# Optimization experiments

Hardware: AMD Instinct MI355X
Metric: run time of the kernel (lower is better)

## Reference

```python
import jax, jax.numpy as jnp
import numpy as np

B, LP, LM = 16, 128, 256      # batch, persona len, msg len
V, E, H = 32000, 512, 512     # vocab, embed dim, lstm units
DENC = 2 * H                  # bidirectional encoder output width


def _glorot(key, shape):
    return jax.random.normal(key, shape, jnp.float32) * (1.0 / np.sqrt(shape[0]))


def setup_inputs() -> dict:
    key = jax.random.key(0)
    ks = jax.random.split(key, 32)
    d = {}
    d["input_word"] = jax.random.randint(ks[0], (B, 1), 0, V)
    d["enc_persona"] = jax.random.normal(ks[1], (B, LP, DENC), jnp.float32)
    d["enc_msg"] = jax.random.normal(ks[2], (B, LM, DENC), jnp.float32)
    d["ctx"] = jax.random.normal(ks[3], (B, 2 * DENC), jnp.float32)
    for i, n in enumerate(["h1", "c1", "h2", "c2", "h3", "c3", "h4", "c4"]):
        d[n] = jax.random.normal(ks[4 + i], (B, H), jnp.float32) * 0.1
    d["emb_table"] = jax.random.normal(ks[12], (V, E), jnp.float32) * 0.02
    in_sizes = [E + 2 * DENC, H, H, H]
    k = 13
    for li, sz in enumerate(in_sizes, start=1):
        d[f"lstm{li}_Wx"] = _glorot(ks[k], (sz, 4 * H)); k += 1
        d[f"lstm{li}_Wh"] = _glorot(ks[k], (H, 4 * H)); k += 1
        d[f"lstm{li}_b"] = jnp.zeros((4 * H,), jnp.float32)
    for pre in ["p", "m"]:
        d[f"{pre}W1_w"] = _glorot(ks[k], (DENC, H)); k += 1
        d[f"{pre}W1_b"] = jnp.zeros((H,), jnp.float32)
        d[f"{pre}W2_w"] = _glorot(ks[k], (H, H)); k += 1
        d[f"{pre}W2_b"] = jnp.zeros((H,), jnp.float32)
        d[f"{pre}V_w"] = _glorot(ks[k], (H, 1)); k += 1
        d[f"{pre}V_b"] = jnp.zeros((1,), jnp.float32)
    d["out_w"] = _glorot(ks[k], (H + 2 * DENC, V)); k += 1
    d["out_b"] = jnp.zeros((V,), jnp.float32)
    return d


def _lstm_step(x, h, c, Wx, Wh, b):
    # Keras LSTM gate order: i, f, g (candidate), o
    z = x @ Wx + h @ Wh + b
    i, f, g, o = jnp.split(z, 4, axis=-1)
    c_new = jax.nn.sigmoid(f) * c + jax.nn.sigmoid(i) * jnp.tanh(g)
    h_new = jax.nn.sigmoid(o) * jnp.tanh(c_new)
    return h_new, c_new


def _bahdanau(enc, dec, W1w, W1b, W2w, W2b, Vw, Vb):
    # enc: [B, L, DENC], dec: [B, 1, H]
    score = jnp.tanh(enc @ W1w + W1b + dec @ W2w + W2b) @ Vw + Vb  # [B, L, 1]
    w = jax.nn.softmax(score, axis=1)
    ctx = jnp.sum(w * enc, axis=1)  # [B, DENC]
    return ctx, w


def reference(input_word, enc_persona, enc_msg, ctx, h1, c1, h2, c2, h3, c3, h4, c4,
              emb_table,
              lstm1_Wx, lstm1_Wh, lstm1_b, lstm2_Wx, lstm2_Wh, lstm2_b,
              lstm3_Wx, lstm3_Wh, lstm3_b, lstm4_Wx, lstm4_Wh, lstm4_b,
              pW1_w, pW1_b, pW2_w, pW2_b, pV_w, pV_b,
              mW1_w, mW1_b, mW2_w, mW2_b, mV_w, mV_b,
              out_w, out_b):
    emb = emb_table[input_word[:, 0]]                 # [B, E]
    x = jnp.concatenate([ctx, emb], axis=-1)          # [B, 2*DENC + E] (seq len 1, squeezed)
    h1, c1 = _lstm_step(x, h1, c1, lstm1_Wx, lstm1_Wh, lstm1_b)
    h2, c2 = _lstm_step(h1, h2, c2, lstm2_Wx, lstm2_Wh, lstm2_b)
    h3, c3 = _lstm_step(h2, h3, c3, lstm3_Wx, lstm3_Wh, lstm3_b)
    h4, c4 = _lstm_step(h3, h4, c4, lstm4_Wx, lstm4_Wh, lstm4_b)
    dec = h4[:, None, :]                              # [B, 1, H]
    p_ctx, p_w = _bahdanau(enc_persona, dec, pW1_w, pW1_b, pW2_w, pW2_b, pV_w, pV_b)
    m_ctx, m_w = _bahdanau(enc_msg, dec, mW1_w, mW1_b, mW2_w, mW2_b, mV_w, mV_b)
    ctx_new = jnp.concatenate([p_ctx, m_ctx], axis=-1)  # [B, 2*DENC]
    # dropout is identity at inference
    logits = jnp.concatenate([h4, ctx_new], axis=-1) @ out_w + out_b  # [B, V]
    return (logits, p_w, m_w, ctx_new, h1, c1, h2, c2, h3, c3, h4, c4)
```

## Files before the change

### kernel.cpp

```cpp
#include <hip/hip_runtime.h>
#include <hip/hip_bf16.h>

#define B 16
#define LP 128
#define LM 256
#define V 32000
#define E 512
#define H 512
#define DENC 1024
#define K1 2560
#define G4 2048

#define OFF_LOGITS 0
#define OFF_PW 512000
#define OFF_MW 514048
#define OFF_CTX 518144
#define OFF_H1 550912
#define OFF_C1 559104
#define OFF_H2 567296
#define OFF_C2 575488
#define OFF_H3 583680
#define OFF_C3 591872
#define OFF_H4 600064
#define OFF_C4 608256

#define ZSPLIT 32
#define LSPLIT 4

#define WS_X      0
#define WS_ZPART  40960
#define WS_D2P    1089536
#define WS_D2M    1097728
#define WS_SP     1105920
#define WS_SM     1107968
#define WS_XXT    1112064
#define WS_LPART  1153024

__device__ __forceinline__ float sigm(float x) { return 1.0f / (1.0f + expf(-x)); }

__global__ void k_embed(const int* __restrict__ word, const float* __restrict__ ctx,
                        const float* __restrict__ emb, float* __restrict__ x)
{
    int b = blockIdx.x;
    int w = word[b];
    for (int i = threadIdx.x; i < 2 * DENC; i += 256) x[b * K1 + i] = ctx[b * 2 * DENC + i];
    for (int i = threadIdx.x; i < E; i += 256)        x[b * K1 + 2 * DENC + i] = emb[(size_t)w * E + i];
}

__global__ void k_lstm_zp(const float* __restrict__ x, int kx,
                          const float* __restrict__ h,
                          const float* __restrict__ Wx, const float* __restrict__ Wh,
                          float* __restrict__ zpart)
{
    int j = blockIdx.x * 256 + threadIdx.x;
    int K = kx + H;
    int chunk = K / ZSPLIT;
    int k0 = blockIdx.y * chunk;
    int k1 = k0 + chunk;

    __shared__ float xs[96 * 16];
    for (int idx = threadIdx.x; idx < chunk * 16; idx += 256) {
        int kk = idx >> 4, b = idx & 15;
        int k = k0 + kk;
        xs[idx] = (k < kx) ? x[b * kx + k] : h[b * H + (k - kx)];
    }
    __syncthreads();

    float acc[16];
    #pragma unroll
    for (int b = 0; b < 16; ++b) acc[b] = 0.f;

    #pragma unroll 4
    for (int k = k0; k < k1; ++k) {
        float w = (k < kx) ? Wx[(size_t)k * G4 + j] : Wh[(size_t)(k - kx) * G4 + j];
        const float4* xp = (const float4*)&xs[(k - k0) * 16];
        float4 x0 = xp[0], x1 = xp[1], x2 = xp[2], x3 = xp[3];
        acc[0]  += x0.x * w; acc[1]  += x0.y * w; acc[2]  += x0.z * w; acc[3]  += x0.w * w;
        acc[4]  += x1.x * w; acc[5]  += x1.y * w; acc[6]  += x1.z * w; acc[7]  += x1.w * w;
        acc[8]  += x2.x * w; acc[9]  += x2.y * w; acc[10] += x2.z * w; acc[11] += x2.w * w;
        acc[12] += x3.x * w; acc[13] += x3.y * w; acc[14] += x3.z * w; acc[15] += x3.w * w;
    }

    float* zp = zpart + (size_t)blockIdx.y * B * G4;
    #pragma unroll
    for (int b = 0; b < 16; ++b) zp[b * G4 + j] = acc[b];
}

__global__ void k_gates(const float* __restrict__ zpart, const float* __restrict__ bias,
                        const float* __restrict__ c_old,
                        float* __restrict__ h_new, float* __restrict__ c_new)
{
    int b = blockIdx.y;
    int j = blockIdx.x * 256 + threadIdx.x;
    float zi = bias[j], zf = bias[H + j], zg = bias[2 * H + j], zo = bias[3 * H + j];
    #pragma unroll
    for (int s = 0; s < ZSPLIT; ++s) {
        const float* zp = zpart + ((size_t)s * B + b) * G4;
        zi += zp[j]; zf += zp[H + j]; zg += zp[2 * H + j]; zo += zp[3 * H + j];
    }
    float c = sigm(zf) * c_old[b * H + j] + sigm(zi) * tanhf(zg);
    float hh = sigm(zo) * tanhf(c);
    c_new[b * H + j] = c;
    h_new[b * H + j] = hh;
}

__global__ void k_decproj(const float* __restrict__ h4,
                          const float* __restrict__ pW2w, const float* __restrict__ pW2b,
                          const float* __restrict__ mW2w, const float* __restrict__ mW2b,
                          float* __restrict__ d2p, float* __restrict__ d2m)
{
    int b = blockIdx.y;
    int j = blockIdx.x * 256 + threadIdx.x;
    int which = blockIdx.z;
    const float* W = which ? mW2w : pW2w;
    const float* bb = which ? mW2b : pW2b;
    float* o = which ? d2m : d2p;
    const float* hr = h4 + b * H;
    float acc = bb[j];
    #pragma unroll 8
    for (int k = 0; k < H; ++k) acc += hr[k] * W[k * H + j];
    o[b * H + j] = acc;
}

#define TL 16
#define CH 128
__global__ void k_attscore(const float* __restrict__ encP, const float* __restrict__ encM,
                           const float* __restrict__ pW1w, const float* __restrict__ pW1b,
                           const float* __restrict__ pVw,  const float* __restrict__ pVb,
                           const float* __restrict__ mW1w, const float* __restrict__ mW1b,
                           const float* __restrict__ mVw,  const float* __restrict__ mVb,
                           const float* __restrict__ d2p,  const float* __restrict__ d2m,
                           float* __restrict__ sp, float* __restrict__ sm)
{
    __shared__ float smem[4352];
    int tile = blockIdx.x, b = blockIdx.y, tid = threadIdx.x;
    const int PT = LP / TL;
    const float *enc, *W1, *W1bv, *Vw, *Vbv, *d2;
    float* sout; int L, l0;
    if (tile < PT) { enc = encP; W1 = pW1w; W1bv = pW1b; Vw = pVw; Vbv = pVb; d2 = d2p; sout = sp; L = LP; l0 = tile * TL; }
    else           { enc = encM; W1 = mW1w; W1bv = mW1b; Vw = mVw; Vbv = mVb; d2 = d2m; sout = sm; L = LM; l0 = (tile - PT) * TL; }

    float accA[TL], accB[TL];
    #pragma unroll
    for (int l = 0; l < TL; ++l) { accA[l] = 0.f; accB[l] = 0.f; }

    for (int kk0 = 0; kk0 < DENC; kk0 += CH) {
        __syncthreads();
        for (int idx = tid; idx < CH * TL; idx += 256) {
            int kk = idx & (CH - 1), ll = idx >> 7;
            smem[kk * 20 + ll] = enc[(size_t)(b * L + l0 + ll) * DENC + kk0 + kk];
        }
        __syncthreads();
        for (int kk = 0; kk < CH; ++kk) {
            float wa = W1[(size_t)(kk0 + kk) * H + tid];
            float wb = W1[(size_t)(kk0 + kk) * H + 256 + tid];
            float el[TL];
            #pragma unroll
            for (int q = 0; q < TL / 4; ++q) {
                float4 t = *(const float4*)&smem[kk * 20 + q * 4];
                el[q * 4 + 0] = t.x; el[q * 4 + 1] = t.y; el[q * 4 + 2] = t.z; el[q * 4 + 3] = t.w;
            }
            #pragma unroll
            for (int l = 0; l < TL; ++l) { accA[l] += el[l] * wa; accB[l] += el[l] * wb; }
        }
    }

    float vA = Vw[tid], vB = Vw[256 + tid];
    float cA = W1bv[tid] + d2[b * H + tid];
    float cB = W1bv[256 + tid] + d2[b * H + 256 + tid];
    float contrib[TL];
    #pragma unroll
    for (int l = 0; l < TL; ++l)
        contrib[l] = tanhf(accA[l] + cA) * vA + tanhf(accB[l] + cB) * vB;

    __syncthreads();
    #pragma unroll
    for (int l = 0; l < TL; ++l) smem[tid * 17 + l] = contrib[l];
    __syncthreads();
    if (tid < TL) {
        float s = Vbv[0];
        for (int t = 0; t < 256; ++t) s += smem[t * 17 + tid];
        sout[b * L + l0 + tid] = s;
    }
}

__global__ void k_softmax(const float* __restrict__ sp, const float* __restrict__ sm,
                          float* __restrict__ out)
{
    int b = blockIdx.x, which = blockIdx.y, tid = threadIdx.x;
    const float* s = which ? sm : sp;
    int L = which ? LM : LP;
    float* wdst = out + (which ? (OFF_MW + b * LM) : (OFF_PW + b * LP));

    __shared__ float red[256];
    float v = (tid < L) ? s[b * L + tid] : -3.4e38f;
    red[tid] = v; __syncthreads();
    for (int off = 128; off > 0; off >>= 1) { if (tid < off) red[tid] = fmaxf(red[tid], red[tid + off]); __syncthreads(); }
    float mx = red[0]; __syncthreads();
    float e = (tid < L) ? expf(v - mx) : 0.f;
    red[tid] = e; __syncthreads();
    for (int off = 128; off > 0; off >>= 1) { if (tid < off) red[tid] += red[tid + off]; __syncthreads(); }
    if (tid < L) wdst[tid] = e / red[0];
}

__global__ void k_ctx(const float* __restrict__ encP, const float* __restrict__ encM,
                      float* __restrict__ out)
{
    int b = blockIdx.y, which = blockIdx.z;
    int d = blockIdx.x * 256 + threadIdx.x;
    const float* enc = which ? encM : encP;
    const float* w = out + (which ? (OFF_MW + b * LM) : (OFF_PW + b * LP));
    int L = which ? LM : LP;
    float acc = 0.f;
    for (int l = 0; l < L; ++l) acc += w[l] * enc[(size_t)(b * L + l) * DENC + d];
    out[OFF_CTX + b * 2 * DENC + which * DENC + d] = acc;
}

__global__ void k_buildxxt(const float* __restrict__ out, float* __restrict__ xxt)
{
    int idx = blockIdx.x * 256 + threadIdx.x;
    int b = idx & 15, k = idx >> 4;
    float v = (k < H) ? out[OFF_H4 + b * H + k]
                      : out[OFF_CTX + b * 2 * DENC + (k - H)];
    xxt[idx] = v;
}

__global__ void k_logits_p(const float* __restrict__ xxt, const float* __restrict__ ow,
                           float* __restrict__ lpart)
{
    int v = blockIdx.x * 256 + threadIdx.x;
    int k0 = blockIdx.y * (K1 / LSPLIT);
    float acc[16];
    #pragma unroll
    for (int b = 0; b < 16; ++b) acc[b] = 0.f;
    #pragma unroll 4
    for (int k = k0; k < k0 + K1 / LSPLIT; ++k) {
        float w = ow[(size_t)k * V + v];
        const float4* xp = (const float4*)&xxt[k * 16];
        float4 x0 = xp[0], x1 = xp[1], x2 = xp[2], x3 = xp[3];
        acc[0]  += x0.x * w; acc[1]  += x0.y * w; acc[2]  += x0.z * w; acc[3]  += x0.w * w;
        acc[4]  += x1.x * w; acc[5]  += x1.y * w; acc[6]  += x1.z * w; acc[7]  += x1.w * w;
        acc[8]  += x2.x * w; acc[9]  += x2.y * w; acc[10] += x2.z * w; acc[11] += x2.w * w;
        acc[12] += x3.x * w; acc[13] += x3.y * w; acc[14] += x3.z * w; acc[15] += x3.w * w;
    }
    #pragma unroll
    for (int b = 0; b < 16; ++b) lpart[((size_t)blockIdx.y * B + b) * V + v] = acc[b];
}

__global__ void k_logits_r(const float* __restrict__ lpart, const float* __restrict__ ob,
                           float* __restrict__ out)
{
    int v = blockIdx.x * 256 + threadIdx.x;
    int b = blockIdx.y;
    float s = ob[v];
    #pragma unroll
    for (int p = 0; p < LSPLIT; ++p) s += lpart[((size_t)p * B + b) * V + v];
    out[(size_t)b * V + v] = s;
}

extern "C" void kernel_launch(void* const* d_in, const int* in_sizes, int n_in,
                              void* d_out, int out_size, void* d_ws, size_t ws_size,
                              hipStream_t stream)
{
    const int*   word = (const int*)d_in[0];
    const float* encP = (const float*)d_in[1];
    const float* encM = (const float*)d_in[2];
    const float* ctx  = (const float*)d_in[3];
    const float* h1o  = (const float*)d_in[4];
    const float* c1o  = (const float*)d_in[5];
    const float* h2o  = (const float*)d_in[6];
    const float* c2o  = (const float*)d_in[7];
    const float* h3o  = (const float*)d_in[8];
    const float* c3o  = (const float*)d_in[9];
    const float* h4o  = (const float*)d_in[10];
    const float* c4o  = (const float*)d_in[11];
    const float* emb  = (const float*)d_in[12];
    const float* Wx1 = (const float*)d_in[13]; const float* Wh1 = (const float*)d_in[14]; const float* b1 = (const float*)d_in[15];
    const float* Wx2 = (const float*)d_in[16]; const float* Wh2 = (const float*)d_in[17]; const float* b2 = (const float*)d_in[18];
    const float* Wx3 = (const float*)d_in[19]; const float* Wh3 = (const float*)d_in[20]; const float* b3 = (const float*)d_in[21];
    const float* Wx4 = (const float*)d_in[22]; const float* Wh4 = (const float*)d_in[23]; const float* b4 = (const float*)d_in[24];
    const float* pW1w = (const float*)d_in[25]; const float* pW1b = (const float*)d_in[26];
    const float* pW2w = (const float*)d_in[27]; const float* pW2b = (const float*)d_in[28];
    const float* pVw  = (const float*)d_in[29]; const float* pVb  = (const float*)d_in[30];
    const float* mW1w = (const float*)d_in[31]; const float* mW1b = (const float*)d_in[32];
    const float* mW2w = (const float*)d_in[33]; const float* mW2b = (const float*)d_in[34];
    const float* mVw  = (const float*)d_in[35]; const float* mVb  = (const float*)d_in[36];
    const float* outw = (const float*)d_in[37]; const float* outb = (const float*)d_in[38];

    float* out = (float*)d_out;
    float* ws  = (float*)d_ws;
    float* X     = ws + WS_X;
    float* ZPART = ws + WS_ZPART;
    float* D2P   = ws + WS_D2P;
    float* D2M   = ws + WS_D2M;
    float* SP    = ws + WS_SP;
    float* SM    = ws + WS_SM;
    float* XXT   = ws + WS_XXT;
    float* LPART = ws + WS_LPART;

    dim3 blk(256);

    k_embed<<<dim3(B), blk, 0, stream>>>(word, ctx, emb, X);

    k_lstm_zp<<<dim3(8, ZSPLIT), blk, 0, stream>>>(X, K1, h1o, Wx1, Wh1, ZPART);
    k_gates  <<<dim3(2, B), blk, 0, stream>>>(ZPART, b1, c1o, out + OFF_H1, out + OFF_C1);

    k_lstm_zp<<<dim3(8, ZSPLIT), blk, 0, stream>>>(out + OFF_H1, H, h2o, Wx2, Wh2, ZPART);
    k_gates  <<<dim3(2, B), blk, 0, stream>>>(ZPART, b2, c2o, out + OFF_H2, out + OFF_C2);

    k_lstm_zp<<<dim3(8, ZSPLIT), blk, 0, stream>>>(out + OFF_H2, H, h3o, Wx3, Wh3, ZPART);
    k_gates  <<<dim3(2, B), blk, 0, stream>>>(ZPART, b3, c3o, out + OFF_H3, out + OFF_C3);

    k_lstm_zp<<<dim3(8, ZSPLIT), blk, 0, stream>>>(out + OFF_H3, H, h4o, Wx4, Wh4, ZPART);
    k_gates  <<<dim3(2, B), blk, 0, stream>>>(ZPART, b4, c4o, out + OFF_H4, out + OFF_C4);

    k_decproj<<<dim3(2, B, 2), blk, 0, stream>>>(out + OFF_H4, pW2w, pW2b, mW2w, mW2b, D2P, D2M);

    k_attscore<<<dim3(LP / TL + LM / TL, B), blk, 0, stream>>>(
        encP, encM, pW1w, pW1b, pVw, pVb, mW1w, mW1b, mVw, mVb, D2P, D2M, SP, SM);

    k_softmax<<<dim3(B, 2), blk, 0, stream>>>(SP, SM, out);
    k_ctx<<<dim3(DENC / 256, B, 2), blk, 0, stream>>>(encP, encM, out);

    k_buildxxt<<<dim3(K1 * B / 256), blk, 0, stream>>>(out, XXT);

    k_logits_p<<<dim3(V / 256, LSPLIT), blk, 0, stream>>>(XXT, outw, LPART);
    k_logits_r<<<dim3(V / 256, B), blk, 0, stream>>>(LPART, outb, out);
}
```

Baseline: 950.3 us.

## Use bf16 MFMA for attention scores, fuse xxt build, raise logits split

Converts the encoder outputs and the transposed W1 weights to bf16 on every call, then computes the attention score projection with 16x16x32 bf16 MFMA instructions instead of scalar FP32 FMAs. The separate xxt build kernel is removed: the gate and context kernels now write their results directly into the transposed logits input. The logits K-split is doubled and loop unroll factors are increased. The change adds conversion passes over the encoder tensors, lowers precision in the score path, and the MFMA kernel launches only 96 blocks.

```diff
diff --git a/kernel.cpp b/kernel.cpp
--- a/kernel.cpp
+++ b/kernel.cpp
@@ -25,7 +25,7 @@
 #define OFF_C4 608256
 
 #define ZSPLIT 32
-#define LSPLIT 4
+#define LSPLIT 8
 
 #define WS_X      0
 #define WS_ZPART  40960
@@ -35,8 +35,53 @@
 #define WS_SM     1107968
 #define WS_XXT    1112064
 #define WS_LPART  1153024
+#define WS_ENCBF  5249024
+#define WS_W1T    8394752
+
+#define ENCM_BF_OFF 2097152
+#define W1TM_OFF    524288
+
+typedef __attribute__((ext_vector_type(8))) short bhalf8;
+typedef __attribute__((ext_vector_type(4))) float f32x4;
 
 __device__ __forceinline__ float sigm(float x) { return 1.0f / (1.0f + expf(-x)); }
+
+__global__ void k_cvt_enc(const float* __restrict__ encP, const float* __restrict__ encM,
+                          __hip_bfloat16* __restrict__ encbf)
+{
+    int which = blockIdx.y;
+    const float* src = which ? encM : encP;
+    __hip_bfloat16* dst = encbf + (which ? ENCM_BF_OFF : 0);
+    int n4 = (which ? B * LM * DENC : B * LP * DENC) / 4;
+    int i = blockIdx.x * 256 + threadIdx.x;
+    if (i < n4) {
+        float4 v = ((const float4*)src)[i];
+        __hip_bfloat16 o[4] = { __float2bfloat16(v.x), __float2bfloat16(v.y),
+                                __float2bfloat16(v.z), __float2bfloat16(v.w) };
+        *(short4*)&dst[i * 4] = *(short4*)o;
+    }
+}
+
+__global__ void k_cvtT(const float* __restrict__ pW1w, const float* __restrict__ mW1w,
+                       __hip_bfloat16* __restrict__ w1t)
+{
+    __shared__ float tile[64][65];
+    int which = blockIdx.z;
+    const float* src = which ? mW1w : pW1w;
+    __hip_bfloat16* dst = w1t + (which ? W1TM_OFF : 0);
+    int k0 = blockIdx.x * 64, j0 = blockIdx.y * 64;
+    for (int it = 0; it < 16; ++it) {
+        int idx = it * 256 + threadIdx.x;
+        int jj = idx & 63, kk = idx >> 6;
+        tile[kk][jj] = src[(size_t)(k0 + kk) * H + j0 + jj];
+    }
+    __syncthreads();
+    for (int it = 0; it < 16; ++it) {
+        int idx = it * 256 + threadIdx.x;
+        int kk = idx & 63, jj = idx >> 6;
+        dst[(size_t)(j0 + jj) * DENC + k0 + kk] = __float2bfloat16(tile[kk][jj]);
+    }
+}
 
 __global__ void k_embed(const int* __restrict__ word, const float* __restrict__ ctx,
                         const float* __restrict__ emb, float* __restrict__ x)
@@ -88,7 +133,8 @@
 
 __global__ void k_gates(const float* __restrict__ zpart, const float* __restrict__ bias,
                         const float* __restrict__ c_old,
-                        float* __restrict__ h_new, float* __restrict__ c_new)
+                        float* __restrict__ h_new, float* __restrict__ c_new,
+                        float* __restrict__ xxt)
 {
     int b = blockIdx.y;
     int j = blockIdx.x * 256 + threadIdx.x;
@@ -102,6 +148,7 @@
     float hh = sigm(zo) * tanhf(c);
     c_new[b * H + j] = c;
     h_new[b * H + j] = hh;
+    if (xxt) xxt[j * 16 + b] = hh;
 }
 
 __global__ void k_decproj(const float* __restrict__ h4,
@@ -122,65 +169,63 @@
     o[b * H + j] = acc;
 }
 
-#define TL 16
-#define CH 128
-__global__ void k_attscore(const float* __restrict__ encP, const float* __restrict__ encM,
-                           const float* __restrict__ pW1w, const float* __restrict__ pW1b,
-                           const float* __restrict__ pVw,  const float* __restrict__ pVb,
-                           const float* __restrict__ mW1w, const float* __restrict__ mW1b,
-                           const float* __restrict__ mVw,  const float* __restrict__ mVb,
-                           const float* __restrict__ d2p,  const float* __restrict__ d2m,
-                           float* __restrict__ sp, float* __restrict__ sm)
-{
-    __shared__ float smem[4352];
-    int tile = blockIdx.x, b = blockIdx.y, tid = threadIdx.x;
-    const int PT = LP / TL;
-    const float *enc, *W1, *W1bv, *Vw, *Vbv, *d2;
-    float* sout; int L, l0;
-    if (tile < PT) { enc = encP; W1 = pW1w; W1bv = pW1b; Vw = pVw; Vbv = pVb; d2 = d2p; sout = sp; L = LP; l0 = tile * TL; }
-    else           { enc = encM; W1 = mW1w; W1bv = mW1b; Vw = mVw; Vbv = mVb; d2 = d2m; sout = sm; L = LM; l0 = (tile - PT) * TL; }
-
-    float accA[TL], accB[TL];
-    #pragma unroll
-    for (int l = 0; l < TL; ++l) { accA[l] = 0.f; accB[l] = 0.f; }
-
-    for (int kk0 = 0; kk0 < DENC; kk0 += CH) {
-        __syncthreads();
-        for (int idx = tid; idx < CH * TL; idx += 256) {
-            int kk = idx & (CH - 1), ll = idx >> 7;
-            smem[kk * 20 + ll] = enc[(size_t)(b * L + l0 + ll) * DENC + kk0 + kk];
+__global__ void k_attscore_mfma(const __hip_bfloat16* __restrict__ encbf,
+                                const __hip_bfloat16* __restrict__ w1t,
+                                const float* __restrict__ pW1b, const float* __restrict__ pVw,
+                                const float* __restrict__ pVb,
+                                const float* __restrict__ mW1b, const float* __restrict__ mVw,
+                                const float* __restrict__ mVb,
+                                const float* __restrict__ d2p, const float* __restrict__ d2m,
+                                float* __restrict__ sp, float* __restrict__ sm)
+{
+    int t = blockIdx.x;
+    int b, lt, L;
+    const __hip_bfloat16 *enc, *wt;
+    const float *w1b, *vw, *vb, *d2;
+    float* sout;
+    if (t < 32) { b = t >> 1; lt = t & 1; L = LP; enc = encbf; wt = w1t;
+                  w1b = pW1b; vw = pVw; vb = pVb; d2 = d2p; sout = sp; }
+    else { int u = t - 32; b = u >> 2; lt = u & 3; L = LM; enc = encbf + ENCM_BF_OFF;
+           wt = w1t + W1TM_OFF; w1b = mW1b; vw = mVw; vb = mVb; d2 = d2m; sout = sm; }
+
+    int wave = threadIdx.x >> 6, lane = threadIdx.x & 63;
+    int m = lane & 15, quad = lane >> 4;
+    int row0 = lt * 64 + wave * 16;
+
+    const __hip_bfloat16* arow = enc + (size_t)(b * L + row0 + m) * DENC + quad * 8;
+
+    f32x4 acc[32];
+    #pragma unroll
+    for (int nt = 0; nt < 32; ++nt) acc[nt] = (f32x4){0.f, 0.f, 0.f, 0.f};
+
+    for (int kt = 0; kt < 32; ++kt) {
+        bhalf8 a = *(const bhalf8*)(arow + kt * 32);
+        #pragma unroll
+        for (int nt = 0; nt < 32; ++nt) {
+            bhalf8 bf = *(const bhalf8*)(wt + (size_t)(nt * 16 + m) * DENC + kt * 32 + quad * 8);
+            acc[nt] = __builtin_amdgcn_mfma_f32_16x16x32_bf16(a, bf, acc[nt], 0, 0, 0);
         }
-        __syncthreads();
-        for (int kk = 0; kk < CH; ++kk) {
-            float wa = W1[(size_t)(kk0 + kk) * H + tid];
-            float wb = W1[(size_t)(kk0 + kk) * H + 256 + tid];
-            float el[TL];
-            #pragma unroll
-            for (int q = 0; q < TL / 4; ++q) {
-                float4 t = *(const float4*)&smem[kk * 20 + q * 4];
-                el[q * 4 + 0] = t.x; el[q * 4 + 1] = t.y; el[q * 4 + 2] = t.z; el[q * 4 + 3] = t.w;
-            }
-            #pragma unroll
-            for (int l = 0; l < TL; ++l) { accA[l] += el[l] * wa; accB[l] += el[l] * wb; }
-        }
-    }
-
-    float vA = Vw[tid], vB = Vw[256 + tid];
-    float cA = W1bv[tid] + d2[b * H + tid];
-    float cB = W1bv[256 + tid] + d2[b * H + 256 + tid];
-    float contrib[TL];
-    #pragma unroll
-    for (int l = 0; l < TL; ++l)
-        contrib[l] = tanhf(accA[l] + cA) * vA + tanhf(accB[l] + cB) * vB;
-
-    __syncthreads();
-    #pragma unroll
-    for (int l = 0; l < TL; ++l) smem[tid * 17 + l] = contrib[l];
-    __syncthreads();
-    if (tid < TL) {
-        float s = Vbv[0];
-        for (int t = 0; t < 256; ++t) s += smem[t * 17 + tid];
-        sout[b * L + l0 + tid] = s;
+    }
+
+    float sacc[4] = {0.f, 0.f, 0.f, 0.f};
+    #pragma unroll
+    for (int nt = 0; nt < 32; ++nt) {
+        int j = nt * 16 + m;
+        float cadd = w1b[j] + d2[b * H + j];
+        float vv = vw[j];
+        #pragma unroll
+        for (int r = 0; r < 4; ++r) sacc[r] += tanhf(acc[nt][r] + cadd) * vv;
+    }
+    #pragma unroll
+    for (int off = 1; off < 16; off <<= 1) {
+        #pragma unroll
+        for (int r = 0; r < 4; ++r) sacc[r] += __shfl_xor(sacc[r], off);
+    }
+    if (m == 0) {
+        float v0 = vb[0];
+        #pragma unroll
+        for (int r = 0; r < 4; ++r)
+            sout[b * L + row0 + quad * 4 + r] = sacc[r] + v0;
     }
 }
 
@@ -204,7 +249,7 @@
 }
 
 __global__ void k_ctx(const float* __restrict__ encP, const float* __restrict__ encM,
-                      float* __restrict__ out)
+                      float* __restrict__ out, float* __restrict__ xxt)
 {
     int b = blockIdx.y, which = blockIdx.z;
     int d = blockIdx.x * 256 + threadIdx.x;
@@ -212,17 +257,10 @@
     const float* w = out + (which ? (OFF_MW + b * LM) : (OFF_PW + b * LP));
     int L = which ? LM : LP;
     float acc = 0.f;
+    #pragma unroll 8
     for (int l = 0; l < L; ++l) acc += w[l] * enc[(size_t)(b * L + l) * DENC + d];
     out[OFF_CTX + b * 2 * DENC + which * DENC + d] = acc;
-}
-
-__global__ void k_buildxxt(const float* __restrict__ out, float* __restrict__ xxt)
-{
-    int idx = blockIdx.x * 256 + threadIdx.x;
-    int b = idx & 15, k = idx >> 4;
-    float v = (k < H) ? out[OFF_H4 + b * H + k]
-                      : out[OFF_CTX + b * 2 * DENC + (k - H)];
-    xxt[idx] = v;
+    xxt[(H + which * DENC + d) * 16 + b] = acc;
 }
 
 __global__ void k_logits_p(const float* __restrict__ xxt, const float* __restrict__ ow,
@@ -233,7 +271,7 @@
     float acc[16];
     #pragma unroll
     for (int b = 0; b < 16; ++b) acc[b] = 0.f;
-    #pragma unroll 4
+    #pragma unroll 8
     for (int k = k0; k < k0 + K1 / LSPLIT; ++k) {
         float w = ow[(size_t)k * V + v];
         const float4* xp = (const float4*)&xxt[k * 16];
@@ -297,32 +335,35 @@
     float* SM    = ws + WS_SM;
     float* XXT   = ws + WS_XXT;
     float* LPART = ws + WS_LPART;
+    __hip_bfloat16* ENCBF = (__hip_bfloat16*)(ws + WS_ENCBF);
+    __hip_bfloat16* W1T   = (__hip_bfloat16*)(ws + WS_W1T);
 
     dim3 blk(256);
 
+    k_cvt_enc<<<dim3((B * LM * DENC / 4 + 255) / 256, 2), blk, 0, stream>>>(encP, encM, ENCBF);
+    k_cvtT<<<dim3(DENC / 64, H / 64, 2), blk, 0, stream>>>(pW1w, mW1w, W1T);
+
     k_embed<<<dim3(B), blk, 0, stream>>>(word, ctx, emb, X);
 
     k_lstm_zp<<<dim3(8, ZSPLIT), blk, 0, stream>>>(X, K1, h1o, Wx1, Wh1, ZPART);
-    k_gates  <<<dim3(2, B), blk, 0, stream>>>(ZPART, b1, c1o, out + OFF_H1, out + OFF_C1);
+    k_gates  <<<dim3(2, B), blk, 0, stream>>>(ZPART, b1, c1o, out + OFF_H1, out + OFF_C1, nullptr);
 
     k_lstm_zp<<<dim3(8, ZSPLIT), blk, 0, stream>>>(out + OFF_H1, H, h2o, Wx2, Wh2, ZPART);
-    k_gates  <<<dim3(2, B), blk, 0, stream>>>(ZPART, b2, c2o, out + OFF_H2, out + OFF_C2);
+    k_gates  <<<dim3(2, B), blk, 0, stream>>>(ZPART, b2, c2o, out + OFF_H2, out + OFF_C2, nullptr);
 
     k_lstm_zp<<<dim3(8, ZSPLIT), blk, 0, stream>>>(out + OFF_H2, H, h3o, Wx3, Wh3, ZPART);
-    k_gates  <<<dim3(2, B), blk, 0, stream>>>(ZPART, b3, c3o, out + OFF_H3, out + OFF_C3);
+    k_gates  <<<dim3(2, B), blk, 0, stream>>>(ZPART, b3, c3o, out + OFF_H3, out + OFF_C3, nullptr);
 
     k_lstm_zp<<<dim3(8, ZSPLIT), blk, 0, stream>>>(out + OFF_H3, H, h4o, Wx4, Wh4, ZPART);
-    k_gates  <<<dim3(2, B), blk, 0, stream>>>(ZPART, b4, c4o, out + OFF_H4, out + OFF_C4);
+    k_gates  <<<dim3(2, B), blk, 0, stream>>>(ZPART, b4, c4o, out + OFF_H4, out + OFF_C4, XXT);
 
     k_decproj<<<dim3(2, B, 2), blk, 0, stream>>>(out + OFF_H4, pW2w, pW2b, mW2w, mW2b, D2P, D2M);
 
-    k_attscore<<<dim3(LP / TL + LM / TL, B), blk, 0, stream>>>(
-        encP, encM, pW1w, pW1b, pVw, pVb, mW1w, mW1b, mVw, mVb, D2P, D2M, SP, SM);
+    k_attscore_mfma<<<dim3(32 + 64), blk, 0, stream>>>(
+        ENCBF, W1T, pW1b, pVw, pVb, mW1b, mVw, mVb, D2P, D2M, SP, SM);
 
     k_softmax<<<dim3(B, 2), blk, 0, stream>>>(SP, SM, out);
-    k_ctx<<<dim3(DENC / 256, B, 2), blk, 0, stream>>>(encP, encM, out);
-
-    k_buildxxt<<<dim3(K1 * B / 256), blk, 0, stream>>>(out, XXT);
+    k_ctx<<<dim3(DENC / 256, B, 2), blk, 0, stream>>>(encP, encM, out, XXT);
 
     k_logits_p<<<dim3(V / 256, LSPLIT), blk, 0, stream>>>(XXT, outw, LPART);
     k_logits_r<<<dim3(V / 256, B), blk, 0, stream>>>(LPART, outb, out);
```

Measured after the change: 1.042 ms. 1.1x slower.
